# Performance work log

Measured on AMD Instinct MI355X. Metric: run time of the kernel, lower is better.

## Reference

```python
import jax, jax.numpy as jnp
import numpy as np

B_SCENES = 2; K = 5; C = 128; H = 64; W = 64
D_INNER = C; D_STATE = 16; DT_RANK = 8
C_TUKEY = 0.3; ALPHA = 2.0; BETA = 0.4; GAMMA = 0.8


def affine_grid(theta, Ho, Wo):
    # torch F.affine_grid, align_corners=False (pixel centers)
    xs = (jnp.arange(Wo, dtype=jnp.float32) + 0.5) * (2.0 / Wo) - 1.0
    ys = (jnp.arange(Ho, dtype=jnp.float32) + 0.5) * (2.0 / Ho) - 1.0
    gx, gy = jnp.meshgrid(xs, ys)
    base = jnp.stack([gx, gy, jnp.ones_like(gx)], axis=-1)  # (H,W,3)
    return jnp.einsum('nij,hwj->nhwi', theta, base)  # (N,H,W,2)


def grid_sample(src, grid):
    # bilinear, zero padding, align_corners=False; src (N,C,H,W), grid (N,H,W,2)
    N, Cc, Hs, Ws = src.shape
    ix = ((grid[..., 0] + 1.0) * Ws - 1.0) * 0.5
    iy = ((grid[..., 1] + 1.0) * Hs - 1.0) * 0.5
    x0 = jnp.floor(ix); y0 = jnp.floor(iy)
    def tap(xf, yf):
        v = ((xf >= 0) & (xf <= Ws - 1) & (yf >= 0) & (yf <= Hs - 1)).astype(src.dtype)
        xc = jnp.clip(xf, 0, Ws - 1).astype(jnp.int32)
        yc = jnp.clip(yf, 0, Hs - 1).astype(jnp.int32)
        vals = jax.vmap(lambda s, y, x: s[:, y, x])(src, yc, xc)  # (N,C,H,W)
        return vals * v[:, None]
    wx1 = (ix - x0)[:, None]; wy1 = (iy - y0)[:, None]
    wx0 = 1.0 - wx1; wy0 = 1.0 - wy1
    return (tap(x0, y0) * wx0 * wy0 + tap(x0 + 1.0, y0) * wx1 * wy0
            + tap(x0, y0 + 1.0) * wx0 * wy1 + tap(x0 + 1.0, y0 + 1.0) * wx1 * wy1)


def ss2d(tokens, in_proj_w, conv_w, conv_b, x_proj_w, dt_w, dt_b, A_logs, Ds, ln_g, ln_b, out_proj_w):
    # tokens (C, Hs, Ws) channel-first; VMamba-style v05_noz core, d_inner=C
    xin = jnp.einsum('chw,dc->dhw', tokens, in_proj_w)
    xc = jax.lax.conv_general_dilated(xin[None], conv_w, (1, 1), [(1, 1), (1, 1)],
                                      dimension_numbers=('NCHW', 'OIHW', 'NCHW'),
                                      feature_group_count=D_INNER)[0] + conv_b[:, None, None]
    xa = jax.nn.silu(xc)
    d, Hs, Ws = xa.shape
    L = Hs * Ws
    x_hw = xa.reshape(d, L)
    x_wh = jnp.swapaxes(xa, 1, 2).reshape(d, L)
    xs = jnp.stack([x_hw, x_wh, x_hw[:, ::-1], x_wh[:, ::-1]], axis=0)  # (4,d,L)
    x_dbl = jnp.einsum('kdl,kcd->kcl', xs, x_proj_w)
    dt = x_dbl[:, :DT_RANK]
    Bm = x_dbl[:, DT_RANK:DT_RANK + D_STATE]
    Cm = x_dbl[:, DT_RANK + D_STATE:]
    dts = jax.nn.softplus(jnp.einsum('kdr,krl->kdl', dt_w, dt) + dt_b[..., None])
    A = -jnp.exp(A_logs)  # (4,d,n)
    seq = (jnp.moveaxis(xs, -1, 0), jnp.moveaxis(dts, -1, 0),
           jnp.moveaxis(Bm, -1, 0), jnp.moveaxis(Cm, -1, 0))
    def step(h, inp):
        xt, dtt, Bt, Ct = inp
        h = h * jnp.exp(dtt[..., None] * A) + (dtt * xt)[..., None] * Bt[:, None, :]
        return h, jnp.einsum('kdn,kn->kd', h, Ct)
    h0 = jnp.zeros((4, d, D_STATE), tokens.dtype)
    _, ys = jax.lax.scan(jax.checkpoint(step), h0, seq)  # ys (L,4,d)
    ys = jnp.moveaxis(ys, 0, -1) + Ds[..., None] * xs  # (4,d,L)
    untr = lambda y: jnp.swapaxes(y.reshape(d, Ws, Hs), 1, 2).reshape(d, L)
    y = ys[0] + untr(ys[1]) + ys[2][:, ::-1] + untr(ys[3][:, ::-1])
    yt = y.T  # (L,d)
    mu = yt.mean(-1, keepdims=True)
    var = ((yt - mu) ** 2).mean(-1, keepdims=True)
    yn = (yt - mu) * jax.lax.rsqrt(var + 1e-5) * ln_g + ln_b
    out = yn @ out_proj_w.T  # (L,C)
    return jnp.moveaxis(out.reshape(Hs, Ws, -1), -1, 0)  # (C,Hs,Ws)


def forward(x, nam, in_proj_w, conv_w, conv_b, x_proj_w, dt_w, dt_b, A_logs, Ds, ln_g, ln_b, out_proj_w):
    xg = x.reshape(B_SCENES, K, C, H, W)  # record_len is constant K
    t_rows = nam[:, 0]  # ego row i=0 of t_matrix: (B,K,2,3)
    def scene(xb, t_row):
        warped = grid_sample(xb, affine_grid(t_row, H, W))  # (K,C,H,W)
        ego = warped[0]
        # per-pixel cosine sim across channels (F.normalize(dim=0) on (C,HW) views)
        en = ego / jnp.maximum(jnp.sqrt((ego ** 2).sum(0, keepdims=True)), 1e-6)
        nb = warped / jnp.maximum(jnp.sqrt((warped ** 2).sum(1, keepdims=True)), 1e-6)
        sims = jnp.clip((en[None] * nb).sum(1), -1.0, 1.0)  # (K,H,W)
        r = jnp.maximum(1.0 - sims, 0.0)
        xr = jnp.maximum(r / C_TUKEY, 0.0)
        w_pix = jnp.maximum(jnp.maximum(1.0 - xr * xr, 0.0) ** 2, 1e-6)[:, None]  # (K,1,H,W)
        tx = t_row[:, 0, 2]; ty = t_row[:, 1, 2]
        yaw = jnp.abs(jnp.arctan2(t_row[:, 0, 1], t_row[:, 0, 0]))
        g = jax.nn.sigmoid(ALPHA - BETA * jnp.sqrt(tx ** 2 + ty ** 2) - GAMMA * yaw)  # (K,)
        logit = jnp.log(w_pix + 1e-8) + jnp.log(g + 1e-8)[:, None, None, None]
        alpha = jax.nn.softmax(logit, axis=0)  # softmax over K per pixel
        weighted = warped * alpha
        tokens = jnp.swapaxes(weighted.reshape(K, C, H * W), 0, 1)  # (C,K,HW)
        out = ss2d(tokens, in_proj_w, conv_w, conv_b, x_proj_w, dt_w, dt_b,
                   A_logs, Ds, ln_g, ln_b, out_proj_w)  # (C,K,HW)
        return jnp.swapaxes(out, 0, 1).reshape(K, C, W, H)[0]  # (C,W,H) as in original view
    return jax.vmap(scene)(xg, t_rows)


def setup_inputs() -> dict:
    key = jax.random.key(0)
    ks = jax.random.split(key, 10)
    x = jax.random.normal(ks[0], (B_SCENES * K, C, H, W), jnp.float32)
    record_len = jnp.full((B_SCENES,), K, dtype=jnp.int32)
    eye = jnp.broadcast_to(jnp.array([[1.0, 0.0, 0.0], [0.0, 1.0, 0.0]], jnp.float32),
                           (B_SCENES, K, K, 2, 3))
    nam = eye + 0.05 * jax.random.normal(ks[1], (B_SCENES, K, K, 2, 3), jnp.float32)
    in_proj_w = 0.05 * jax.random.normal(ks[2], (D_INNER, C), jnp.float32)
    conv_w = 0.1 * jax.random.normal(ks[3], (D_INNER, 1, 3, 3), jnp.float32)
    conv_b = jnp.zeros((D_INNER,), jnp.float32)
    x_proj_w = 0.05 * jax.random.normal(ks[4], (4, DT_RANK + 2 * D_STATE, D_INNER), jnp.float32)
    dt_w = 0.1 * jax.random.normal(ks[5], (4, D_INNER, DT_RANK), jnp.float32)
    dt_b = -4.6 + 0.5 * jax.random.normal(ks[6], (4, D_INNER), jnp.float32)
    A_logs = jnp.broadcast_to(jnp.log(jnp.arange(1, D_STATE + 1, dtype=jnp.float32)),
                              (4, D_INNER, D_STATE)) + jnp.zeros((4, D_INNER, D_STATE), jnp.float32)
    Ds = jnp.ones((4, D_INNER), jnp.float32)
    ln_g = jnp.ones((D_INNER,), jnp.float32)
    ln_b = jnp.zeros((D_INNER,), jnp.float32)
    out_proj_w = 0.05 * jax.random.normal(ks[7], (C, D_INNER), jnp.float32)
    return {"x": x, "record_len": record_len, "normalized_affine_matrix": nam,
            "in_proj_w": in_proj_w, "conv_w": conv_w, "conv_b": conv_b,
            "x_proj_w": x_proj_w, "dt_w": dt_w, "dt_b": dt_b, "A_logs": A_logs,
            "Ds": Ds, "ln_g": ln_g, "ln_b": ln_b, "out_proj_w": out_proj_w}


def reference(x, record_len, normalized_affine_matrix, in_proj_w, conv_w, conv_b,
              x_proj_w, dt_w, dt_b, A_logs, Ds, ln_g, ln_b, out_proj_w):
    # record_len is a constant (= K per scene) and only determines the static grouping
    return forward(x, normalized_affine_matrix, in_proj_w, conv_w, conv_b,
                   x_proj_w, dt_w, dt_b, A_logs, Ds, ln_g, ln_b, out_proj_w)
```

## Files before the change

### kernel.cpp

```cpp
#include <hip/hip_runtime.h>
#include <math.h>

#define B_S   2
#define PIX   4096
#define LL    20480
#define NS    16
#define RR    8
#define NCHK  256
#define LC    80
#define SUBS  16
#define NSUB  5
#define NGRP  16
#define GCH   16
#define K0CP  26

typedef float v2f __attribute__((ext_vector_type(2)));

__device__ __forceinline__ v2f pk_mul(v2f a, v2f b) {
  v2f d;
  asm("v_pk_mul_f32 %0, %1, %2" : "=v"(d) : "v"(a), "v"(b));
  return d;
}
#define PK_FMA_ACC(a, b, c) asm("v_pk_fma_f32 %0, %1, %2, %0" : "+v"(a) : "v"(b), "v"(c))
#define PK_DECAY(h, e, m) asm("v_pk_fma_f32 %0, %0, %1, %2" : "+v"(h) : "v"(e), "v"(m))

template<int K>
__device__ __forceinline__ int zmapT(int l) {
  if (K == 0) return l;
  if (K == 1) return ((l % 5) << 12) + l / 5;
  if (K == 2) return 20479 - l;
  int lr = 20479 - l;
  return ((lr % 5) << 12) + lr / 5;
}

__global__ __launch_bounds__(256)
void k_warp(const float* __restrict__ x, const float* __restrict__ nam,
            float* __restrict__ warped) {
  int g = blockIdx.x * 256 + threadIdx.x;
  int p  = g & 4095;
  int c  = (g >> 12) & 127;
  int bk = g >> 19;
  int b = bk / 5, k = bk - b * 5;
  const float* th = nam + (size_t)(b * 25 + k) * 6;
  float gx = ((p & 63) + 0.5f) * 0.03125f - 1.0f;
  float gy = ((p >> 6) + 0.5f) * 0.03125f - 1.0f;
  float grx = th[0] * gx + th[1] * gy + th[2];
  float gry = th[3] * gx + th[4] * gy + th[5];
  float ix = ((grx + 1.0f) * 64.0f - 1.0f) * 0.5f;
  float iy = ((gry + 1.0f) * 64.0f - 1.0f) * 0.5f;
  float x0 = floorf(ix), y0 = floorf(iy);
  float fx = ix - x0,  fy = iy - y0;
  const float* src = x + (size_t)(bk * 128 + c) * PIX;
  float acc = 0.0f;
  #pragma unroll
  for (int dy = 0; dy < 2; ++dy) {
    float yf = y0 + dy;
    float wy = dy ? fy : 1.0f - fy;
    if (yf < 0.0f || yf > 63.0f) continue;
    int yi = (int)yf;
    #pragma unroll
    for (int dx = 0; dx < 2; ++dx) {
      float xf = x0 + dx;
      float wx = dx ? fx : 1.0f - fx;
      if (xf < 0.0f || xf > 63.0f) continue;
      acc += wx * wy * src[yi * 64 + (int)xf];
    }
  }
  warped[g] = acc;
}

__global__ __launch_bounds__(512)
void k_alpha(const float* __restrict__ warped, const float* __restrict__ nam,
             float* __restrict__ alpha) {
  __shared__ float part[8][64][9];
  int blk = blockIdx.x;
  int b = blk >> 6;
  int p0 = (blk & 63) << 6;
  int wv = threadIdx.x >> 6, lane = threadIdx.x & 63;
  int p = p0 + lane;
  const float* wb = warped + (size_t)b * 5 * 128 * PIX + p;
  float dot[5] = {0,0,0,0,0}, ssq[5] = {0,0,0,0,0};
  int c0 = wv * 16;
  for (int c = c0; c < c0 + 16; ++c) {
    float w0 = wb[(size_t)c * PIX];
    ssq[0] += w0 * w0;
    #pragma unroll
    for (int k = 1; k < 5; ++k) {
      float wk = wb[((size_t)k * 128 + c) * PIX];
      dot[k] += w0 * wk;
      ssq[k] += wk * wk;
    }
  }
  part[wv][lane][0] = ssq[0];
  #pragma unroll
  for (int k = 1; k < 5; ++k) {
    part[wv][lane][k] = dot[k];
    part[wv][lane][4 + k] = ssq[k];
  }
  __syncthreads();
  if (threadIdx.x < 64) {
    float q[9];
    #pragma unroll
    for (int j = 0; j < 9; ++j) {
      float s = 0.0f;
      #pragma unroll
      for (int w = 0; w < 8; ++w) s += part[w][lane][j];
      q[j] = s;
    }
    float n0 = fmaxf(sqrtf(q[0]), 1e-6f);
    float logit[5];
    #pragma unroll
    for (int k = 0; k < 5; ++k) {
      float dotk = (k == 0) ? q[0] : q[k];
      float ssqk = (k == 0) ? q[0] : q[4 + k];
      float nk = fmaxf(sqrtf(ssqk), 1e-6f);
      float sim = fminf(fmaxf(dotk / (n0 * nk), -1.0f), 1.0f);
      float r = fmaxf(1.0f - sim, 0.0f);
      float xr = r * (1.0f / 0.3f);
      float tt = fmaxf(1.0f - xr * xr, 0.0f);
      float wp = fmaxf(tt * tt, 1e-6f);
      const float* th = nam + (size_t)(b * 25 + k) * 6;
      float tx = th[2], ty = th[5];
      float yaw = fabsf(atan2f(th[1], th[0]));
      float gk = 1.0f / (1.0f + __expf(-(2.0f - 0.4f * sqrtf(tx*tx + ty*ty) - 0.8f * yaw)));
      logit[k] = __logf(wp + 1e-8f) + __logf(gk + 1e-8f);
    }
    float m = logit[0];
    #pragma unroll
    for (int k = 1; k < 5; ++k) m = fmaxf(m, logit[k]);
    float e[5], s = 0.0f;
    #pragma unroll
    for (int k = 0; k < 5; ++k) { e[k] = __expf(logit[k] - m); s += e[k]; }
    float inv = 1.0f / s;
    #pragma unroll
    for (int k = 0; k < 5; ++k)
      alpha[((size_t)(b * 5 + k)) * PIX + p] = e[k] * inv;
  }
}

__global__ __launch_bounds__(256, 4)
void k_gemm_in(const float* __restrict__ warped, const float* __restrict__ alpha,
               const float* __restrict__ W, float* __restrict__ X0) {
  __shared__ float xl[64][129];
  __shared__ __align__(16) float wlT[32][132];
  int t = threadIdx.x;
  int row0 = blockIdx.x * 64;
  int b = row0 / LL;
  int z0 = row0 - b * LL;
  int a = z0 >> 12;
  int p0 = z0 & 4095;
  int ba = b * 5 + a;
  int r = t & 63, cg = t >> 6;
  float av = alpha[(size_t)ba * PIX + p0 + r];
  #pragma unroll
  for (int i = 0; i < 32; ++i) {
    int c = cg * 32 + i;
    xl[r][c] = warped[((size_t)ba * 128 + c) * PIX + p0 + r] * av;
  }
  int zl = t & 63, mg = t >> 6;
  float acc[32];
  #pragma unroll
  for (int i = 0; i < 32; ++i) acc[i] = 0.0f;
  for (int c0 = 0; c0 < 128; c0 += 32) {
    __syncthreads();
    #pragma unroll
    for (int i = 0; i < 16; ++i) {
      int m = (t >> 5) * 16 + i;
      wlT[t & 31][m] = W[(size_t)m * 128 + c0 + (t & 31)];
    }
    __syncthreads();
    for (int cc = 0; cc < 32; ++cc) {
      float xv = xl[zl][c0 + cc];
      const float4* wr = (const float4*)(&wlT[cc][mg * 32]);
      #pragma unroll
      for (int q = 0; q < 8; ++q) {
        float4 w4 = wr[q];
        acc[q*4+0] = fmaf(w4.x, xv, acc[q*4+0]);
        acc[q*4+1] = fmaf(w4.y, xv, acc[q*4+1]);
        acc[q*4+2] = fmaf(w4.z, xv, acc[q*4+2]);
        acc[q*4+3] = fmaf(w4.w, xv, acc[q*4+3]);
      }
    }
  }
  __syncthreads();
  #pragma unroll
  for (int q = 0; q < 32; ++q) xl[zl][mg * 32 + q] = acc[q];
  __syncthreads();
  #pragma unroll
  for (int i = 0; i < 32; ++i) {
    int idx = i * 256 + t;
    X0[((size_t)row0 + (idx >> 7)) * 128 + (idx & 127)] = xl[idx >> 7][idx & 127];
  }
}

__global__ __launch_bounds__(256)
void k_conv(const float* __restrict__ X0, const float* __restrict__ cw,
            const float* __restrict__ cb, float* __restrict__ XT) {
  int g = blockIdx.x * 256 + threadIdx.x;
  int d = g & 127;
  int zz4 = g >> 7;
  int b = zz4 / (LL / 4);
  int r = zz4 - b * (LL / 4);
  int z0 = r * 4;
  int a = z0 >> 12, p = z0 & 4095;
  float w9[9];
  #pragma unroll
  for (int i = 0; i < 9; ++i) w9[i] = cw[d * 9 + i];
  float cbv = cb[d];
  float acc[4] = {cbv, cbv, cbv, cbv};
  #pragma unroll
  for (int di = 0; di < 3; ++di) {
    int aa = a + di - 1;
    if (aa < 0 || aa >= 5) continue;
    const float* rowb = X0 + ((size_t)b * LL + (size_t)aa * PIX) * 128 + d;
    #pragma unroll
    for (int dj = -1; dj <= 4; ++dj) {
      int pp = p + dj;
      if (pp < 0 || pp >= PIX) continue;
      float v = rowb[(size_t)pp * 128];
      #pragma unroll
      for (int o = 0; o < 4; ++o) {
        int rel = dj - o;
        if (rel >= -1 && rel <= 1) acc[o] = fmaf(w9[di * 3 + rel + 1], v, acc[o]);
      }
    }
  }
  float* dst = XT + (size_t)(zz4 * 4) * 128 + d;
  #pragma unroll
  for (int o = 0; o < 4; ++o) {
    float sg = 1.0f / (1.0f + __expf(-acc[o]));
    dst[(size_t)o * 128] = acc[o] * sg;
  }
}

__global__ __launch_bounds__(256, 4)
void k_gemmZ(const float* __restrict__ X, const float* __restrict__ W,
             float* __restrict__ ZdtB, float* __restrict__ ZC) {
  __shared__ float xl[64][129];
  __shared__ __align__(16) float wlT[32][164];
  int t = threadIdx.x;
  int row0 = blockIdx.x * 64;
  #pragma unroll
  for (int i = 0; i < 32; ++i) {
    int idx = i * 256 + t;
    xl[idx >> 7][idx & 127] = X[((size_t)row0 + (idx >> 7)) * 128 + (idx & 127)];
  }
  int zl = t & 63, mg = t >> 6;
  float acc[40];
  #pragma unroll
  for (int i = 0; i < 40; ++i) acc[i] = 0.0f;
  for (int c0 = 0; c0 < 128; c0 += 32) {
    __syncthreads();
    #pragma unroll
    for (int i = 0; i < 20; ++i) {
      int m = (t >> 5) * 20 + i;
      wlT[t & 31][m] = W[(size_t)m * 128 + c0 + (t & 31)];
    }
    __syncthreads();
    for (int cc = 0; cc < 32; ++cc) {
      float xv = xl[zl][c0 + cc];
      const float4* wr = (const float4*)(&wlT[cc][mg * 40]);
      #pragma unroll
      for (int q = 0; q < 10; ++q) {
        float4 w4 = wr[q];
        acc[q*4+0] = fmaf(w4.x, xv, acc[q*4+0]);
        acc[q*4+1] = fmaf(w4.y, xv, acc[q*4+1]);
        acc[q*4+2] = fmaf(w4.z, xv, acc[q*4+2]);
        acc[q*4+3] = fmaf(w4.w, xv, acc[q*4+3]);
      }
    }
  }
  int row = row0 + zl;
  int b = row / LL, z = row - b * LL;
  int a = z >> 12, qq = z & 4095;
  int l;
  if (mg == 0)      l = z;
  else if (mg == 1) l = 5 * qq + a;
  else if (mg == 2) l = 20479 - z;
  else              l = 20479 - (5 * qq + a);
  float* dD = ZdtB + ((size_t)(b * 4 + mg) * LL + l) * 24;
  #pragma unroll
  for (int q2 = 0; q2 < 6; ++q2) {
    float4 v = make_float4(acc[q2*4], acc[q2*4+1], acc[q2*4+2], acc[q2*4+3]);
    *(float4*)(dD + q2 * 4) = v;
  }
  float* dC = ZC + ((size_t)(b * 4 + mg) * LL + l) * 16;
  #pragma unroll
  for (int q2 = 0; q2 < 4; ++q2) {
    float4 v = make_float4(acc[24+q2*4], acc[24+q2*4+1], acc[24+q2*4+2], acc[24+q2*4+3]);
    *(float4*)(dC + q2 * 4) = v;
  }
}

template<int K>
__device__ void scan_body(int b, int chunk, int dh, int lane,
    const float* __restrict__ XT, const float* __restrict__ ZdtB,
    const float* __restrict__ ZC,
    const float* __restrict__ dt_w, const float* __restrict__ dt_b,
    const float* __restrict__ A_logs, const float* __restrict__ Ds,
    float* __restrict__ h_out, float* __restrict__ sumdts,
    float* __restrict__ ysz, float* __restrict__ cumdtv,
    float* stD, float* stC, float* xs)
{
  const int d = dh * 64 + lane;
  const int kd = K * 128 + d;
  bool chainok = true;
  #pragma unroll
  for (int n = 0; n < NS; ++n) {
    float An = -__expf(A_logs[(size_t)kd * 16 + n]);
    chainok = chainok && (fabsf(An + (float)(n + 1)) < 3e-5f * (float)(n + 1));
  }
  v2f dw2[4];
  #pragma unroll
  for (int r = 0; r < 4; ++r) {
    dw2[r][0] = dt_w[(size_t)kd * 8 + 2 * r];
    dw2[r][1] = dt_w[(size_t)kd * 8 + 2 * r + 1];
  }
  const float dtb = dt_b[kd], dsv = Ds[kd];
  v2f h2[8];
  #pragma unroll
  for (int n = 0; n < 8; ++n) h2[n] = (v2f){0.0f, 0.0f};
  float sdt = 0.0f;
  const int seq = b * 4 + K;
  const float* ZDs = ZdtB + (size_t)seq * LL * 24;
  const float* ZCs = ZC + (size_t)seq * LL * 16;
  const float* Xb = XT + (size_t)b * LL * 128;
  float* ysb = ysz + (size_t)seq * PIX * 128;
  float* cdb = cumdtv + (size_t)seq * PIX * 128;
  const int l0 = chunk * LC;

  if (__all(chainok ? 1 : 0)) {
    #pragma unroll 1
    for (int sub = 0; sub < NSUB; ++sub) {
      const int ls = l0 + sub * SUBS;
      {
        const v2f* srcD = (const v2f*)(ZDs + (size_t)ls * 24);
        v2f* dstD = (v2f*)stD;
        #pragma unroll
        for (int i = 0; i < 3; ++i) dstD[i * 64 + lane] = srcD[i * 64 + lane];
      }
      int s0c = 0;
      bool needC;
      if (K == 0)      needC = (ls < PIX);
      else if (K == 2) needC = (ls + SUBS > LL - PIX);
      else             needC = true;
      if (K == 1) s0c = (5 - (ls % 5)) % 5;
      if (K == 3) s0c = (9 - (ls % 5)) % 5;
      if (needC) {
        if (K == 0 || K == 2) {
          const v2f* srcC = (const v2f*)(ZCs + (size_t)ls * 16);
          v2f* dstC = (v2f*)stC;
          #pragma unroll
          for (int i = 0; i < 2; ++i) dstC[i * 64 + lane] = srcC[i * 64 + lane];
        } else {
          int j = lane >> 4, col = lane & 15;
          int l = ls + s0c + 5 * j;
          if (l > LL - 1) l = LL - 1;
          stC[lane] = ZCs[(size_t)l * 16 + col];
        }
      }
      #pragma unroll
      for (int s = 0; s < SUBS; ++s) {
        int z = zmapT<K>(ls + s);
        xs[s * 64 + lane] = Xb[(size_t)z * 128 + d];
      }
      int zc = 0;
      if (K == 1) zc = (ls + s0c) / 5;
      if (K == 3) zc = (20479 - ls - s0c) / 5;
      int yj = 0;
      #pragma unroll
      for (int s = 0; s < SUBS; ++s) {
        const v2f* rowD = (const v2f*)(stD + s * 24);
        v2f zd0 = rowD[0], zd1 = rowD[1], zd2 = rowD[2], zd3 = rowD[3];
        v2f da = pk_mul(dw2[0], zd0);
        PK_FMA_ACC(da, dw2[1], zd1);
        PK_FMA_ACC(da, dw2[2], zd2);
        PK_FMA_ACC(da, dw2[3], zd3);
        float dtl = dtb + da[0] + da[1];
        float edt = __expf(dtl);
        float e1 = __builtin_amdgcn_rcpf(1.0f + edt);
        float dt = (dtl > 20.0f) ? dtl : __logf(1.0f + edt);
        sdt += dt;
        float xsv = xs[s * 64 + lane];
        float dtx = dt * xsv;
        v2f dtx2 = {dtx, dtx};
        float e2 = e1 * e1;
        v2f E[8];
        E[0] = (v2f){e1, e2};
        v2f e2s = {e2, e2};
        E[1] = pk_mul(E[0], e2s);
        E[2] = pk_mul(E[1], e2s);
        E[3] = pk_mul(E[2], e2s);
        float e8 = E[3][1];
        v2f e8s = {e8, e8};
        E[4] = pk_mul(E[0], e8s);
        E[5] = pk_mul(E[1], e8s);
        E[6] = pk_mul(E[2], e8s);
        E[7] = pk_mul(E[3], e8s);
        const v2f* B2 = (const v2f*)(stD + s * 24 + 8);
        #pragma unroll
        for (int i = 0; i < 8; ++i) {
          v2f m = pk_mul(dtx2, B2[i]);
          PK_DECAY(h2[i], E[i], m);
        }
        bool doY;
        int z;
        if (K == 0)      { z = ls + s;            doY = (z < PIX); }
        else if (K == 2) { z = 20479 - (ls + s);  doY = (z < PIX); }
        else             { z = zc;                doY = ((s % 5) == s0c); }
        if (doY) {
          const v2f* C2 = (const v2f*)(stC + ((K == 0 || K == 2) ? s : yj) * 16);
          v2f ya = pk_mul(h2[0], C2[0]);
          #pragma unroll
          for (int i = 1; i < 8; ++i) PK_FMA_ACC(ya, h2[i], C2[i]);
          float y = fmaf(dsv, xsv, ya[0] + ya[1]);
          size_t o = (size_t)z * 128 + d;
          ysb[o] = y;
          cdb[o] = sdt;
          ++yj;
          if (K == 1) ++zc;
          if (K == 3) --zc;
        }
      }
    }
  } else {
    float An[NS];
    #pragma unroll
    for (int n = 0; n < NS; ++n) An[n] = -__expf(A_logs[(size_t)kd * 16 + n]);
    float hs[NS];
    #pragma unroll
    for (int n = 0; n < NS; ++n) hs[n] = 0.0f;
    #pragma unroll 1
    for (int l = l0; l < l0 + LC; ++l) {
      int z = zmapT<K>(l);
      const float* rowD = ZDs + (size_t)l * 24;
      float dtl = dtb;
      #pragma unroll
      for (int r = 0; r < RR; ++r) dtl += dt_w[(size_t)kd * 8 + r] * rowD[r];
      float edt = __expf(dtl);
      float dt = (dtl > 20.0f) ? dtl : __logf(1.0f + edt);
      sdt += dt;
      float xv = Xb[(size_t)z * 128 + d];
      float dtx = dt * xv;
      #pragma unroll
      for (int n = 0; n < NS; ++n)
        hs[n] = hs[n] * __expf(dt * An[n]) + dtx * rowD[8 + n];
      if (z < PIX) {
        const float* rowC = ZCs + (size_t)l * 16;
        float y = dsv * xv;
        #pragma unroll
        for (int n = 0; n < NS; ++n) y = fmaf(hs[n], rowC[n], y);
        size_t o = (size_t)z * 128 + d;
        ysb[o] = y;
        cdb[o] = sdt;
      }
    }
    #pragma unroll
    for (int n = 0; n < 8; ++n) h2[n] = (v2f){hs[2*n], hs[2*n+1]};
  }
  float* ho = h_out + (((size_t)seq * NCHK + chunk) * 128 + d) * 16;
  #pragma unroll
  for (int n = 0; n < 8; ++n) {
    ho[2*n] = h2[n][0];
    ho[2*n+1] = h2[n][1];
  }
  sumdts[((size_t)seq * NCHK + chunk) * 128 + d] = sdt;
}

__global__ __launch_bounds__(256, 5)
void k_scan1(const float* __restrict__ XT, const float* __restrict__ ZdtB,
             const float* __restrict__ ZC,
             const float* __restrict__ dt_w, const float* __restrict__ dt_b,
             const float* __restrict__ A_logs, const float* __restrict__ Ds,
             float* __restrict__ h_out, float* __restrict__ sumdts,
             float* __restrict__ ysz, float* __restrict__ cumdtv) {
  __shared__ __align__(16) float stD_all[4][SUBS * 24];
  __shared__ __align__(16) float stC_all[4][SUBS * 16];
  __shared__ __align__(16) float xs_all[4][SUBS * 64];
  int tid = threadIdx.x, wid = tid >> 6, lane = tid & 63;
  int bid = blockIdx.x;
  int bb = bid / (K0CP + 384);
  int idx = bid - bb * (K0CP + 384);
  int k, cp;
  if (idx < K0CP)            { k = 0; cp = idx; }
  else if (idx < K0CP + 128) { k = 1; cp = idx - K0CP; }
  else if (idx < K0CP + 256) { k = 2; cp = idx - (K0CP + 128); }
  else                       { k = 3; cp = idx - (K0CP + 256); }
  int chunk = cp * 2 + (wid >> 1);
  int dh = wid & 1;
  float* stD = stD_all[wid];
  float* stC = stC_all[wid];
  float* xs  = xs_all[wid];
  switch (k) {
    case 0: scan_body<0>(bb, chunk, dh, lane, XT, ZdtB, ZC, dt_w, dt_b, A_logs, Ds, h_out, sumdts, ysz, cumdtv, stD, stC, xs); break;
    case 1: scan_body<1>(bb, chunk, dh, lane, XT, ZdtB, ZC, dt_w, dt_b, A_logs, Ds, h_out, sumdts, ysz, cumdtv, stD, stC, xs); break;
    case 2: scan_body<2>(bb, chunk, dh, lane, XT, ZdtB, ZC, dt_w, dt_b, A_logs, Ds, h_out, sumdts, ysz, cumdtv, stD, stC, xs); break;
    default: scan_body<3>(bb, chunk, dh, lane, XT, ZdtB, ZC, dt_w, dt_b, A_logs, Ds, h_out, sumdts, ysz, cumdtv, stD, stC, xs); break;
  }
}

__global__ __launch_bounds__(256)
void k_comb_a(const float* __restrict__ A_logs, const float* __restrict__ sumdts,
              const float* __restrict__ h_out, float* __restrict__ Ag,
              float* __restrict__ Bg) {
  int g = blockIdx.x * 256 + threadIdx.x;
  int n = g & 15;
  int d = (g >> 4) & 127;
  int grp = (g >> 11) & 15;
  int seq = g >> 15;
  int k = seq & 3;
  float An = -__expf(A_logs[(size_t)(k * 128 + d) * 16 + n]);
  float A = 1.0f, Bv = 0.0f;
  size_t cbase = (size_t)seq * NCHK + grp * GCH;
  #pragma unroll 4
  for (int j = 0; j < GCH; ++j) {
    float a = __expf(An * sumdts[(cbase + j) * 128 + d]);
    float b = h_out[((cbase + j) * 128 + d) * 16 + n];
    A *= a;
    Bv = Bv * a + b;
  }
  size_t o = (((size_t)seq * NGRP + grp) * 128 + d) * 16 + n;
  Ag[o] = A;
  Bg[o] = Bv;
}

__global__ __launch_bounds__(256)
void k_comb_b(const float* __restrict__ Ag, const float* __restrict__ Bg,
              float* __restrict__ Hg) {
  int g = blockIdx.x * 256 + threadIdx.x;
  int n = g & 15;
  int d = (g >> 4) & 127;
  int seq = g >> 11;
  float H = 0.0f;
  #pragma unroll
  for (int grp = 0; grp < NGRP; ++grp) {
    size_t o = (((size_t)seq * NGRP + grp) * 128 + d) * 16 + n;
    Hg[o] = H;
    H = Ag[o] * H + Bg[o];
  }
}

__global__ __launch_bounds__(256)
void k_comb_c(const float* __restrict__ A_logs, const float* __restrict__ sumdts,
              const float* __restrict__ h_out, const float* __restrict__ Hg,
              float* __restrict__ h_in) {
  int g = blockIdx.x * 256 + threadIdx.x;
  int n = g & 15;
  int d = (g >> 4) & 127;
  int grp = (g >> 11) & 15;
  int seq = g >> 15;
  int k = seq & 3;
  float An = -__expf(A_logs[(size_t)(k * 128 + d) * 16 + n]);
  float h = Hg[(((size_t)seq * NGRP + grp) * 128 + d) * 16 + n];
  size_t cbase = (size_t)seq * NCHK + grp * GCH;
  #pragma unroll 4
  for (int j = 0; j < GCH; ++j) {
    size_t o = ((cbase + j) * 128 + d) * 16 + n;
    h_in[o] = h;
    float a = __expf(An * sumdts[(cbase + j) * 128 + d]);
    h = a * h + h_out[o];
  }
}

__global__ __launch_bounds__(256)
void k_wt(const float* __restrict__ Wo, float* __restrict__ WT) {
  __shared__ float tl[32][33];
  int bx = blockIdx.x & 3, by = blockIdx.x >> 2;
  int t = threadIdx.x;
  int tx = t & 31, ty = t >> 5;
  #pragma unroll
  for (int i = 0; i < 4; ++i)
    tl[ty + i * 8][tx] = Wo[(size_t)(by * 32 + ty + i * 8) * 128 + bx * 32 + tx];
  __syncthreads();
  #pragma unroll
  for (int i = 0; i < 4; ++i)
    WT[(size_t)(bx * 32 + ty + i * 8) * 128 + by * 32 + tx] = tl[tx][ty + i * 8];
}

__global__ __launch_bounds__(256)
void k_merge(const float* __restrict__ ysz, const float* __restrict__ ZC,
             const float* __restrict__ A_logs, const float* __restrict__ h_in,
             const float* __restrict__ cumdt,
             const float* __restrict__ ln_g, const float* __restrict__ ln_b,
             const float* __restrict__ WT, float* __restrict__ out) {
  __shared__ __align__(16) float ynT[128][20];
  __shared__ float red[4][8][2];
  int blk = blockIdx.x;
  int b = blk >> 8;
  int p0 = (blk & 255) * 16;
  int tid = threadIdx.x;
  int t = tid & 127;
  int half = tid >> 7;
  int w = tid >> 6;
  float g = ln_g[t], bb = ln_b[t];
  bool cok[4];
  #pragma unroll
  for (int k = 0; k < 4; ++k) {
    bool c = true;
    #pragma unroll
    for (int n = 0; n < NS; ++n) {
      float An = -__expf(A_logs[(size_t)(k * 128 + t) * 16 + n]);
      c = c && (fabsf(An + (float)(n + 1)) < 3e-5f * (float)(n + 1));
    }
    cok[k] = c;
  }
  float yv[8];
  #pragma unroll
  for (int i = 0; i < 8; ++i) {
    int p = p0 + 2 * i + half;
    float y = 0.0f;
    #pragma unroll
    for (int k = 0; k < 4; ++k) {
      size_t zi = ((size_t)(b * 4 + k) * PIX + p) * 128 + t;
      float yk = ysz[zi];
      int l;
      if (k == 0)      l = p;
      else if (k == 1) l = 5 * p;
      else if (k == 2) l = 20479 - p;
      else             l = 20479 - 5 * p;
      int chunk = l / LC;
      float cd = cumdt[zi];
      const v2f* hi2 = (const v2f*)(h_in + (((size_t)(b * 4 + k) * NCHK + chunk) * 128 + t) * 16);
      const v2f* Cr2 = (const v2f*)(ZC + ((size_t)(b * 4 + k) * LL + l) * 16);
      float fix;
      if (cok[k]) {
        float q = __expf(-cd);
        float q2 = q * q;
        v2f Q[8];
        Q[0] = (v2f){q, q2};
        v2f q2s = {q2, q2};
        Q[1] = pk_mul(Q[0], q2s);
        Q[2] = pk_mul(Q[1], q2s);
        Q[3] = pk_mul(Q[2], q2s);
        float q8 = Q[3][1];
        v2f q8s = {q8, q8};
        Q[4] = pk_mul(Q[0], q8s);
        Q[5] = pk_mul(Q[1], q8s);
        Q[6] = pk_mul(Q[2], q8s);
        Q[7] = pk_mul(Q[3], q8s);
        v2f a = pk_mul(pk_mul(hi2[0], Cr2[0]), Q[0]);
        #pragma unroll
        for (int j = 1; j < 8; ++j) {
          v2f m = pk_mul(hi2[j], Cr2[j]);
          PK_FMA_ACC(a, m, Q[j]);
        }
        fix = a[0] + a[1];
      } else {
        fix = 0.0f;
        const float* hi = (const float*)hi2;
        const float* Cr = (const float*)Cr2;
        #pragma unroll
        for (int n = 0; n < NS; ++n) {
          float An = -__expf(A_logs[(size_t)(k * 128 + t) * 16 + n]);
          fix += Cr[n] * hi[n] * __expf(An * cd);
        }
      }
      y += yk + fix;
    }
    yv[i] = y;
    float s1 = y, s2 = y * y;
    #pragma unroll
    for (int off = 32; off; off >>= 1) {
      s1 += __shfl_xor(s1, off);
      s2 += __shfl_xor(s2, off);
    }
    if ((tid & 63) == 0) { red[w][i][0] = s1; red[w][i][1] = s2; }
  }
  __syncthreads();
  #pragma unroll
  for (int i = 0; i < 8; ++i) {
    int pl = 2 * i + half;
    float S1 = red[half * 2][i][0] + red[half * 2 + 1][i][0];
    float S2 = red[half * 2][i][1] + red[half * 2 + 1][i][1];
    float mu = S1 * (1.0f / 128.0f);
    float var = S2 * (1.0f / 128.0f) - mu * mu;
    float rs = rsqrtf(var + 1e-5f);
    ynT[t][pl] = (yv[i] - mu) * rs * g + bb;
  }
  __syncthreads();
  float acc[8];
  #pragma unroll
  for (int i = 0; i < 8; ++i) acc[i] = 0.0f;
  for (int dd = 0; dd < 128; ++dd) {
    float wv = WT[(size_t)dd * 128 + t];
    const float4* yr = (const float4*)(&ynT[dd][half * 8]);
    float4 ya = yr[0], yb4 = yr[1];
    acc[0] = fmaf(ya.x,  wv, acc[0]);
    acc[1] = fmaf(ya.y,  wv, acc[1]);
    acc[2] = fmaf(ya.z,  wv, acc[2]);
    acc[3] = fmaf(ya.w,  wv, acc[3]);
    acc[4] = fmaf(yb4.x, wv, acc[4]);
    acc[5] = fmaf(yb4.y, wv, acc[5]);
    acc[6] = fmaf(yb4.z, wv, acc[6]);
    acc[7] = fmaf(yb4.w, wv, acc[7]);
  }
  float* dst = out + ((size_t)b * 128 + t) * PIX + p0 + half * 8;
  float4 v0 = make_float4(acc[0], acc[1], acc[2], acc[3]);
  float4 v1 = make_float4(acc[4], acc[5], acc[6], acc[7]);
  *(float4*)(dst) = v0;
  *(float4*)(dst + 4) = v1;
}

extern "C" void kernel_launch(void* const* d_in, const int* in_sizes, int n_in,
                              void* d_out, int out_size, void* d_ws, size_t ws_size,
                              hipStream_t stream) {
  const float* x         = (const float*)d_in[0];
  const float* nam       = (const float*)d_in[2];
  const float* in_proj_w = (const float*)d_in[3];
  const float* conv_w    = (const float*)d_in[4];
  const float* conv_b    = (const float*)d_in[5];
  const float* x_proj_w  = (const float*)d_in[6];
  const float* dt_w      = (const float*)d_in[7];
  const float* dt_b      = (const float*)d_in[8];
  const float* A_logs    = (const float*)d_in[9];
  const float* Ds        = (const float*)d_in[10];
  const float* ln_g      = (const float*)d_in[11];
  const float* ln_b      = (const float*)d_in[12];
  const float* out_proj_w= (const float*)d_in[13];
  float* out = (float*)d_out;
  float* ws  = (float*)d_ws;

  float* warped = ws;
  float* alpha  = warped + 5242880;
  float* X0     = alpha  + 40960;
  float* XT     = X0     + 5242880;
  float* ZdtB   = XT     + 5242880;
  float* ZC     = ZdtB   + 3932160;
  float* sums   = ZC     + 2621440;
  float* ysz    = sums   + 262144;
  float* cumdt  = ysz    + 4194304;
  float* WT     = cumdt  + 4194304;
  float* Ag     = WT     + 16384;
  float* Bg     = Ag     + 262144;
  float* Hg     = Bg     + 262144;

  float* h_out = warped;
  float* h_in  = X0;

  k_warp   <<<20480, 256, 0, stream>>>(x, nam, warped);
  k_alpha  <<<128,   512, 0, stream>>>(warped, nam, alpha);
  k_gemm_in<<<640,   256, 0, stream>>>(warped, alpha, in_proj_w, X0);
  k_conv   <<<5120,  256, 0, stream>>>(X0, conv_w, conv_b, XT);
  k_gemmZ  <<<640,   256, 0, stream>>>(XT, x_proj_w, ZdtB, ZC);
  k_scan1  <<<2 * (K0CP + 384), 256, 0, stream>>>(XT, ZdtB, ZC, dt_w, dt_b,
                                                  A_logs, Ds, h_out, sums, ysz, cumdt);
  k_comb_a <<<1024,  256, 0, stream>>>(A_logs, sums, h_out, Ag, Bg);
  k_comb_b <<<64,    256, 0, stream>>>(Ag, Bg, Hg);
  k_comb_c <<<1024,  256, 0, stream>>>(A_logs, sums, h_out, Hg, h_in);
  k_wt     <<<16,    256, 0, stream>>>(out_proj_w, WT);
  k_merge  <<<512,   256, 0, stream>>>(ysz, ZC, A_logs, h_in, cumdt,
                                       ln_g, ln_b, WT, out);
}
```

Before: 286.0 us.

## Halve scan chunk length, retile projection GEMMs, raise scan occupancy

Scan chunks drop from 80 to 40 steps, so twice as many chunks and combine groups run. This exposes more parallel work in the chunked selective scan and its combine kernels. Both projection GEMMs now give each thread two rows and half the output columns, which reuses each LDS weight load across two rows. The scan's launch bounds rise to 6 waves per SIMD, and the workspace aliases are moved to fit the larger intermediate h and sum buffers. The cost is a larger cross-chunk combine, more intermediate traffic, and tighter register limits in the scan.

```diff
diff --git a/kernel.cpp b/kernel.cpp
--- a/kernel.cpp
+++ b/kernel.cpp
@@ -6,13 +6,13 @@
 #define LL    20480
 #define NS    16
 #define RR    8
-#define NCHK  256
-#define LC    80
-#define SUBS  16
-#define NSUB  5
-#define NGRP  16
+#define NCHK  512
+#define LC    40
+#define SUBS  10
+#define NSUB  4
+#define NGRP  32
 #define GCH   16
-#define K0CP  26
+#define K0CP  52
 
 typedef float v2f __attribute__((ext_vector_type(2)));
 
@@ -157,10 +157,11 @@
     int c = cg * 32 + i;
     xl[r][c] = warped[((size_t)ba * 128 + c) * PIX + p0 + r] * av;
   }
-  int zl = t & 63, mg = t >> 6;
-  float acc[32];
-  #pragma unroll
-  for (int i = 0; i < 32; ++i) acc[i] = 0.0f;
+  int zl2 = t & 31;
+  int mg  = t >> 5;
+  float acc0[16], acc1[16];
+  #pragma unroll
+  for (int i = 0; i < 16; ++i) { acc0[i] = 0.0f; acc1[i] = 0.0f; }
   for (int c0 = 0; c0 < 128; c0 += 32) {
     __syncthreads();
     #pragma unroll
@@ -169,22 +170,32 @@
       wlT[t & 31][m] = W[(size_t)m * 128 + c0 + (t & 31)];
     }
     __syncthreads();
+    const float* xr0 = xl[2 * zl2];
+    const float* xr1 = xl[2 * zl2 + 1];
     for (int cc = 0; cc < 32; ++cc) {
-      float xv = xl[zl][c0 + cc];
-      const float4* wr = (const float4*)(&wlT[cc][mg * 32]);
-      #pragma unroll
-      for (int q = 0; q < 8; ++q) {
+      float xv0 = xr0[c0 + cc];
+      float xv1 = xr1[c0 + cc];
+      const float4* wr = (const float4*)(&wlT[cc][mg * 16]);
+      #pragma unroll
+      for (int q = 0; q < 4; ++q) {
         float4 w4 = wr[q];
-        acc[q*4+0] = fmaf(w4.x, xv, acc[q*4+0]);
-        acc[q*4+1] = fmaf(w4.y, xv, acc[q*4+1]);
-        acc[q*4+2] = fmaf(w4.z, xv, acc[q*4+2]);
-        acc[q*4+3] = fmaf(w4.w, xv, acc[q*4+3]);
+        acc0[q*4+0] = fmaf(w4.x, xv0, acc0[q*4+0]);
+        acc0[q*4+1] = fmaf(w4.y, xv0, acc0[q*4+1]);
+        acc0[q*4+2] = fmaf(w4.z, xv0, acc0[q*4+2]);
+        acc0[q*4+3] = fmaf(w4.w, xv0, acc0[q*4+3]);
+        acc1[q*4+0] = fmaf(w4.x, xv1, acc1[q*4+0]);
+        acc1[q*4+1] = fmaf(w4.y, xv1, acc1[q*4+1]);
+        acc1[q*4+2] = fmaf(w4.z, xv1, acc1[q*4+2]);
+        acc1[q*4+3] = fmaf(w4.w, xv1, acc1[q*4+3]);
       }
     }
   }
   __syncthreads();
   #pragma unroll
-  for (int q = 0; q < 32; ++q) xl[zl][mg * 32 + q] = acc[q];
+  for (int q = 0; q < 16; ++q) {
+    xl[2 * zl2][mg * 16 + q] = acc0[q];
+    xl[2 * zl2 + 1][mg * 16 + q] = acc1[q];
+  }
   __syncthreads();
   #pragma unroll
   for (int i = 0; i < 32; ++i) {
@@ -245,10 +256,11 @@
     int idx = i * 256 + t;
     xl[idx >> 7][idx & 127] = X[((size_t)row0 + (idx >> 7)) * 128 + (idx & 127)];
   }
-  int zl = t & 63, mg = t >> 6;
-  float acc[40];
-  #pragma unroll
-  for (int i = 0; i < 40; ++i) acc[i] = 0.0f;
+  int zl2 = t & 31;
+  int mg  = t >> 5;
+  float acc0[20], acc1[20];
+  #pragma unroll
+  for (int i = 0; i < 20; ++i) { acc0[i] = 0.0f; acc1[i] = 0.0f; }
   for (int c0 = 0; c0 < 128; c0 += 32) {
     __syncthreads();
     #pragma unroll
@@ -257,38 +269,53 @@
       wlT[t & 31][m] = W[(size_t)m * 128 + c0 + (t & 31)];
     }
     __syncthreads();
+    const float* xr0 = xl[2 * zl2];
+    const float* xr1 = xl[2 * zl2 + 1];
     for (int cc = 0; cc < 32; ++cc) {
-      float xv = xl[zl][c0 + cc];
-      const float4* wr = (const float4*)(&wlT[cc][mg * 40]);
-      #pragma unroll
-      for (int q = 0; q < 10; ++q) {
+      float xv0 = xr0[c0 + cc];
+      float xv1 = xr1[c0 + cc];
+      const float4* wr = (const float4*)(&wlT[cc][mg * 20]);
+      #pragma unroll
+      for (int q = 0; q < 5; ++q) {
         float4 w4 = wr[q];
-        acc[q*4+0] = fmaf(w4.x, xv, acc[q*4+0]);
-        acc[q*4+1] = fmaf(w4.y, xv, acc[q*4+1]);
-        acc[q*4+2] = fmaf(w4.z, xv, acc[q*4+2]);
-        acc[q*4+3] = fmaf(w4.w, xv, acc[q*4+3]);
-      }
-    }
-  }
-  int row = row0 + zl;
-  int b = row / LL, z = row - b * LL;
-  int a = z >> 12, qq = z & 4095;
-  int l;
-  if (mg == 0)      l = z;
-  else if (mg == 1) l = 5 * qq + a;
-  else if (mg == 2) l = 20479 - z;
-  else              l = 20479 - (5 * qq + a);
-  float* dD = ZdtB + ((size_t)(b * 4 + mg) * LL + l) * 24;
-  #pragma unroll
-  for (int q2 = 0; q2 < 6; ++q2) {
-    float4 v = make_float4(acc[q2*4], acc[q2*4+1], acc[q2*4+2], acc[q2*4+3]);
-    *(float4*)(dD + q2 * 4) = v;
-  }
-  float* dC = ZC + ((size_t)(b * 4 + mg) * LL + l) * 16;
-  #pragma unroll
-  for (int q2 = 0; q2 < 4; ++q2) {
-    float4 v = make_float4(acc[24+q2*4], acc[24+q2*4+1], acc[24+q2*4+2], acc[24+q2*4+3]);
-    *(float4*)(dC + q2 * 4) = v;
+        acc0[q*4+0] = fmaf(w4.x, xv0, acc0[q*4+0]);
+        acc0[q*4+1] = fmaf(w4.y, xv0, acc0[q*4+1]);
+        acc0[q*4+2] = fmaf(w4.z, xv0, acc0[q*4+2]);
+        acc0[q*4+3] = fmaf(w4.w, xv0, acc0[q*4+3]);
+        acc1[q*4+0] = fmaf(w4.x, xv1, acc1[q*4+0]);
+        acc1[q*4+1] = fmaf(w4.y, xv1, acc1[q*4+1]);
+        acc1[q*4+2] = fmaf(w4.z, xv1, acc1[q*4+2]);
+        acc1[q*4+3] = fmaf(w4.w, xv1, acc1[q*4+3]);
+      }
+    }
+  }
+  int dir = mg >> 1;
+  int halfc = mg & 1;
+  #pragma unroll
+  for (int rr = 0; rr < 2; ++rr) {
+    const float* acc = rr ? acc1 : acc0;
+    int row = row0 + 2 * zl2 + rr;
+    int b = row / LL, z = row - b * LL;
+    int a = z >> 12, qq = z & 4095;
+    int l;
+    if (dir == 0)      l = z;
+    else if (dir == 1) l = 5 * qq + a;
+    else if (dir == 2) l = 20479 - z;
+    else               l = 20479 - (5 * qq + a);
+    size_t seqrow = (size_t)(b * 4 + dir) * LL + l;
+    if (halfc == 0) {
+      float* dD = ZdtB + seqrow * 24;
+      #pragma unroll
+      for (int q2 = 0; q2 < 5; ++q2)
+        *(float4*)(dD + q2 * 4) = make_float4(acc[q2*4], acc[q2*4+1], acc[q2*4+2], acc[q2*4+3]);
+    } else {
+      float* dD = ZdtB + seqrow * 24;
+      *(float4*)(dD + 20) = make_float4(acc[0], acc[1], acc[2], acc[3]);
+      float* dC = ZC + seqrow * 16;
+      #pragma unroll
+      for (int q2 = 0; q2 < 4; ++q2)
+        *(float4*)(dC + q2 * 4) = make_float4(acc[4+q2*4], acc[4+q2*4+1], acc[4+q2*4+2], acc[4+q2*4+3]);
+    }
   }
 }
 
@@ -337,7 +364,10 @@
         const v2f* srcD = (const v2f*)(ZDs + (size_t)ls * 24);
         v2f* dstD = (v2f*)stD;
         #pragma unroll
-        for (int i = 0; i < 3; ++i) dstD[i * 64 + lane] = srcD[i * 64 + lane];
+        for (int i = 0; i < 2; ++i) {
+          int idx = i * 64 + lane;
+          if (idx < SUBS * 12) dstD[idx] = srcD[idx];
+        }
       }
       int s0c = 0;
       bool needC;
@@ -351,12 +381,17 @@
           const v2f* srcC = (const v2f*)(ZCs + (size_t)ls * 16);
           v2f* dstC = (v2f*)stC;
           #pragma unroll
-          for (int i = 0; i < 2; ++i) dstC[i * 64 + lane] = srcC[i * 64 + lane];
+          for (int i = 0; i < 2; ++i) {
+            int idx = i * 64 + lane;
+            if (idx < SUBS * 8) dstC[idx] = srcC[idx];
+          }
         } else {
           int j = lane >> 4, col = lane & 15;
-          int l = ls + s0c + 5 * j;
-          if (l > LL - 1) l = LL - 1;
-          stC[lane] = ZCs[(size_t)l * 16 + col];
+          if (j < 2) {
+            int l = ls + s0c + 5 * j;
+            if (l > LL - 1) l = LL - 1;
+            stC[lane] = ZCs[(size_t)l * 16 + col];
+          }
         }
       }
       #pragma unroll
@@ -467,7 +502,7 @@
   sumdts[((size_t)seq * NCHK + chunk) * 128 + d] = sdt;
 }
 
-__global__ __launch_bounds__(256, 5)
+__global__ __launch_bounds__(256, 6)
 void k_scan1(const float* __restrict__ XT, const float* __restrict__ ZdtB,
              const float* __restrict__ ZC,
              const float* __restrict__ dt_w, const float* __restrict__ dt_b,
@@ -479,13 +514,13 @@
   __shared__ __align__(16) float xs_all[4][SUBS * 64];
   int tid = threadIdx.x, wid = tid >> 6, lane = tid & 63;
   int bid = blockIdx.x;
-  int bb = bid / (K0CP + 384);
-  int idx = bid - bb * (K0CP + 384);
+  int bb = bid / (K0CP + 768);
+  int idx = bid - bb * (K0CP + 768);
   int k, cp;
   if (idx < K0CP)            { k = 0; cp = idx; }
-  else if (idx < K0CP + 128) { k = 1; cp = idx - K0CP; }
-  else if (idx < K0CP + 256) { k = 2; cp = idx - (K0CP + 128); }
-  else                       { k = 3; cp = idx - (K0CP + 256); }
+  else if (idx < K0CP + 256) { k = 1; cp = idx - K0CP; }
+  else if (idx < K0CP + 512) { k = 2; cp = idx - (K0CP + 256); }
+  else                       { k = 3; cp = idx - (K0CP + 512); }
   int chunk = cp * 2 + (wid >> 1);
   int dh = wid & 1;
   float* stD = stD_all[wid];
@@ -506,8 +541,8 @@
   int g = blockIdx.x * 256 + threadIdx.x;
   int n = g & 15;
   int d = (g >> 4) & 127;
-  int grp = (g >> 11) & 15;
-  int seq = g >> 15;
+  int grp = (g >> 11) & 31;
+  int seq = g >> 16;
   int k = seq & 3;
   float An = -__expf(A_logs[(size_t)(k * 128 + d) * 16 + n]);
   float A = 1.0f, Bv = 0.0f;
@@ -547,8 +582,8 @@
   int g = blockIdx.x * 256 + threadIdx.x;
   int n = g & 15;
   int d = (g >> 4) & 127;
-  int grp = (g >> 11) & 15;
-  int seq = g >> 15;
+  int grp = (g >> 11) & 31;
+  int seq = g >> 16;
   int k = seq & 3;
   float An = -__expf(A_logs[(size_t)(k * 128 + d) * 16 + n]);
   float h = Hg[(((size_t)seq * NGRP + grp) * 128 + d) * 16 + n];
@@ -695,10 +730,8 @@
     acc[7] = fmaf(yb4.w, wv, acc[7]);
   }
   float* dst = out + ((size_t)b * 128 + t) * PIX + p0 + half * 8;
-  float4 v0 = make_float4(acc[0], acc[1], acc[2], acc[3]);
-  float4 v1 = make_float4(acc[4], acc[5], acc[6], acc[7]);
-  *(float4*)(dst) = v0;
-  *(float4*)(dst + 4) = v1;
+  *(float4*)(dst)     = make_float4(acc[0], acc[1], acc[2], acc[3]);
+  *(float4*)(dst + 4) = make_float4(acc[4], acc[5], acc[6], acc[7]);
 }
 
 extern "C" void kernel_launch(void* const* d_in, const int* in_sizes, int n_in,
@@ -727,26 +760,26 @@
   float* ZdtB   = XT     + 5242880;
   float* ZC     = ZdtB   + 3932160;
   float* sums   = ZC     + 2621440;
-  float* ysz    = sums   + 262144;
+  float* ysz    = sums   + 524288;
   float* cumdt  = ysz    + 4194304;
   float* WT     = cumdt  + 4194304;
   float* Ag     = WT     + 16384;
-  float* Bg     = Ag     + 262144;
-  float* Hg     = Bg     + 262144;
-
-  float* h_out = warped;
-  float* h_in  = X0;
+  float* Bg     = Ag     + 524288;
+  float* Hg     = Bg     + 524288;
+
+  float* h_out = ws;
+  float* h_in  = XT;
 
   k_warp   <<<20480, 256, 0, stream>>>(x, nam, warped);
   k_alpha  <<<128,   512, 0, stream>>>(warped, nam, alpha);
   k_gemm_in<<<640,   256, 0, stream>>>(warped, alpha, in_proj_w, X0);
   k_conv   <<<5120,  256, 0, stream>>>(X0, conv_w, conv_b, XT);
   k_gemmZ  <<<640,   256, 0, stream>>>(XT, x_proj_w, ZdtB, ZC);
-  k_scan1  <<<2 * (K0CP + 384), 256, 0, stream>>>(XT, ZdtB, ZC, dt_w, dt_b,
-                                                  A_logs, Ds, h_out, sums, ysz, cumdt);
-  k_comb_a <<<1024,  256, 0, stream>>>(A_logs, sums, h_out, Ag, Bg);
+  k_scan1  <<<B_S * (K0CP + 768), 256, 0, stream>>>(XT, ZdtB, ZC, dt_w, dt_b,
+                                                    A_logs, Ds, h_out, sums, ysz, cumdt);
+  k_comb_a <<<2048,  256, 0, stream>>>(A_logs, sums, h_out, Ag, Bg);
   k_comb_b <<<64,    256, 0, stream>>>(Ag, Bg, Hg);
-  k_comb_c <<<1024,  256, 0, stream>>>(A_logs, sums, h_out, Hg, h_in);
+  k_comb_c <<<2048,  256, 0, stream>>>(A_logs, sums, h_out, Hg, h_in);
   k_wt     <<<16,    256, 0, stream>>>(out_proj_w, WT);
   k_merge  <<<512,   256, 0, stream>>>(ysz, ZC, A_logs, h_in, cumdt,
                                        ln_g, ln_b, WT, out);
```

Measured after the change: 256.8 us. -10.2%, faster.
